# Kernel optimization log

Hardware: AMD Instinct MI355X
Metric: run time of the kernel (lower is better)

The kernel has to match this reference:

```python
import jax, jax.numpy as jnp
import numpy as np

N_NODES = 100000
N_EDGES = 1600000
N_GRAPHS = 64
VOCAB = 50000
D = 128
EPS = 1e-5


def setup_inputs() -> dict:
    key = jax.random.key(0)
    ks = jax.random.split(key, 24)
    tokens = jax.random.randint(ks[0], (N_NODES,), 0, VOCAB)
    src = jax.random.randint(ks[1], (N_EDGES,), 0, N_NODES)
    dst = jax.random.randint(ks[2], (N_EDGES,), 0, N_NODES)
    graph_ids = jnp.sort(jax.random.randint(ks[3], (N_NODES,), 0, N_GRAPHS))
    s = 1.0 / np.sqrt(D)
    inp = {
        'tokens': tokens, 'src': src, 'dst': dst, 'graph_ids': graph_ids,
        'embed': jax.random.normal(ks[4], (VOCAB, D), jnp.float32),
        'W1': jax.random.normal(ks[5], (D, D), jnp.float32) * s,
        'b1': jnp.zeros((D,), jnp.float32),
        'g1': jnp.ones((D,), jnp.float32), 'be1': jnp.zeros((D,), jnp.float32),
        'W2': jax.random.normal(ks[6], (D, D), jnp.float32) * s,
        'b2': jnp.zeros((D,), jnp.float32),
        'g2': jnp.ones((D,), jnp.float32), 'be2': jnp.zeros((D,), jnp.float32),
        'W3': jax.random.normal(ks[7], (D, D), jnp.float32) * s,
        'b3': jnp.zeros((D,), jnp.float32),
        'g3': jnp.ones((D,), jnp.float32), 'be3': jnp.zeros((D,), jnp.float32),
        'fcW1': jax.random.normal(ks[8], (D, D // 2), jnp.float32) * s,
        'fcb1': jnp.zeros((D // 2,), jnp.float32),
        'fcW2': jax.random.normal(ks[9], (D // 2, 2), jnp.float32) * (1.0 / np.sqrt(D // 2)),
        'fcb2': jnp.zeros((2,), jnp.float32),
    }
    return inp


def _graph_conv(h, src, dst, norm_src, norm_dst, W, b):
    # DGL GraphConv, norm='both': D_out^{-1/2} -> sum-aggregate -> D_in^{-1/2} -> linear
    msg = (h * norm_src[:, None])[src]                      # [E, D]
    agg = jax.ops.segment_sum(msg, dst, num_segments=N_NODES)
    return (agg * norm_dst[:, None]) @ W + b


def _bn_relu(h, gamma, beta):
    mu = jnp.mean(h, axis=0)
    var = jnp.mean((h - mu) ** 2, axis=0)                   # biased var (torch BN)
    return jax.nn.relu((h - mu) * jax.lax.rsqrt(var + EPS) * gamma + beta)


def reference(tokens, src, dst, graph_ids, embed,
              W1, b1, g1, be1, W2, b2, g2, be2, W3, b3, g3, be3,
              fcW1, fcb1, fcW2, fcb2):
    ones_e = jnp.ones((N_EDGES,), jnp.float32)
    deg_out = jnp.maximum(jax.ops.segment_sum(ones_e, src, num_segments=N_NODES), 1.0)
    deg_in = jnp.maximum(jax.ops.segment_sum(ones_e, dst, num_segments=N_NODES), 1.0)
    norm_src = jax.lax.rsqrt(deg_out)
    norm_dst = jax.lax.rsqrt(deg_in)

    h = embed[tokens]                                        # [N, D]
    h = _bn_relu(_graph_conv(h, src, dst, norm_src, norm_dst, W1, b1), g1, be1)
    h = _bn_relu(_graph_conv(h, src, dst, norm_src, norm_dst, W2, b2), g2, be2)
    h = _bn_relu(_graph_conv(h, src, dst, norm_src, norm_dst, W3, b3), g3, be3)

    # dgl.mean_nodes per graph
    sums = jax.ops.segment_sum(h, graph_ids, num_segments=N_GRAPHS)  # [G, D]
    cnts = jnp.maximum(jax.ops.segment_sum(jnp.ones((N_NODES,), jnp.float32), graph_ids, num_segments=N_GRAPHS), 1.0)
    hg = sums / cnts[:, None]

    hg = jax.nn.relu(hg @ fcW1 + fcb1)                       # dropout = identity (eval)
    return hg @ fcW2 + fcb2                                  # [G, 2]
```

## Files before the change

### kernel.cpp

```cpp
#include <hip/hip_runtime.h>

#define N_NODES 100000
#define N_EDGES 1600000
#define N_GRAPHS 64
#define DIM 128
#define BN_EPS 1e-5f
#define EPAD 2000000

#define NB_DEG 6250
#define NB_EMB 6250
#define NB_SENT 977
#define NB_WPREP 192
#define NB_HIST 391
#define NBUCK 782
#define NG (NBUCK * NB_HIST)
#define NB_SCANG 1195
#define BUCK_RESERVE 388

#define AT_STRIDE 136

typedef unsigned short ushort_t;
typedef unsigned char uchar_t;
typedef unsigned int uint_t;
typedef __attribute__((ext_vector_type(8))) short bf16x8;
typedef __attribute__((ext_vector_type(4))) float f32x4;

__device__ __forceinline__ float bfl(uint_t u) {
    union { uint_t i; float f; } v; v.i = u << 16; return v.f;
}
__device__ __forceinline__ float bfh(uint_t u) {
    union { uint_t i; float f; } v; v.i = u & 0xffff0000u; return v.f;
}
__device__ __forceinline__ ushort_t f2bf(float f) {
    union { float f; uint_t i; } v; v.f = f;
    uint_t x = v.i;
    return (ushort_t)((x + 0x7fffu + ((x >> 16) & 1u)) >> 16);
}
__device__ __forceinline__ uint_t pack2(float lo, float hi) {
    return ((uint_t)f2bf(hi) << 16) | (uint_t)f2bf(lo);
}

__global__ void k_zero(int* __restrict__ p, int n) {
    int i = blockIdx.x * blockDim.x + threadIdx.x;
    if (i < n) p[i] = 0;
}

__global__ void k_front(const int* __restrict__ src, const int* __restrict__ dst,
                        int* __restrict__ dego,
                        const int* __restrict__ tokens, const float* __restrict__ embed,
                        ushort_t* __restrict__ bufH, ushort_t* __restrict__ bufA,
                        int* __restrict__ esrc,
                        const float* __restrict__ w1, const float* __restrict__ w2,
                        const float* __restrict__ w3, ushort_t* __restrict__ wbt,
                        int* __restrict__ G) {
    __shared__ int hh[NBUCK];
    int b = blockIdx.x;
    int t = threadIdx.x;
    if (b < NB_DEG) {
        int e = b * 256 + t;
        if (e < N_EDGES) atomicAdd(&dego[src[e]], 1);
        return;
    }
    b -= NB_DEG;
    if (b < NB_EMB) {
        int gid = b * 256 + t;
        int node = gid >> 4, sub = gid & 15;
        const float* ep = embed + (size_t)tokens[node] * DIM + sub * 8;
        float4 a = *(const float4*)ep;
        float4 c = *(const float4*)(ep + 4);
        uint4 o;
        o.x = pack2(a.x, a.y); o.y = pack2(a.z, a.w);
        o.z = pack2(c.x, c.y); o.w = pack2(c.z, c.w);
        *(uint4*)(bufH + (size_t)node * DIM + sub * 8) = o;
        return;
    }
    b -= NB_EMB;
    if (b < NB_SENT) {
        int i0 = (b * 256 + t) * 8;
        int4 sv = make_int4(N_NODES, N_NODES, N_NODES, N_NODES);
        if (i0 + 8 <= EPAD) {
            *(int4*)(esrc + i0) = sv;
            *(int4*)(esrc + i0 + 4) = sv;
        } else {
            for (int i = i0; i < EPAD; ++i) esrc[i] = N_NODES;
        }
        if (b == 0 && t < 64)
            ((uint_t*)(bufA + (size_t)N_NODES * DIM))[t] = 0u;
        return;
    }
    b -= NB_SENT;
    if (b < NB_WPREP) {
        int i = b * 256 + t;
        int l = i >> 14;
        int idx = i & (DIM * DIM - 1);
        int n = idx >> 7, k = idx & (DIM - 1);
        const float* wsrc = (l == 0) ? w1 : (l == 1) ? w2 : w3;
        wbt[i] = f2bf(wsrc[k * DIM + n]);
        return;
    }
    b -= NB_WPREP;
    {
        for (int k = t; k < NBUCK; k += 256) hh[k] = 0;
        __syncthreads();
        int e0 = b * 4096;
        int e1 = min(e0 + 4096, N_EDGES);
        for (int i = e0 + t; i < e1; i += 256) atomicAdd(&hh[dst[i] >> 7], 1);
        __syncthreads();
        for (int k = t; k < NBUCK; k += 256) G[k * NB_HIST + b] = hh[k];
    }
}

__global__ void k_scanA(const int* __restrict__ G, int* __restrict__ Gs,
                        int* __restrict__ partials) {
    __shared__ int s[256];
    int t = threadIdx.x;
    int i = blockIdx.x * 256 + t;
    int v = (i < NG) ? G[i] : 0;
    s[t] = v;
    __syncthreads();
    for (int off = 1; off < 256; off <<= 1) {
        int add = (t >= off) ? s[t - off] : 0;
        __syncthreads();
        s[t] += add;
        __syncthreads();
    }
    if (i < NG) Gs[i + 1] = s[t];
    if (t == 255) partials[blockIdx.x] = s[t];
}

__global__ void k_scanB(const int* __restrict__ partials, int* __restrict__ Gs) {
    __shared__ int s[256];
    int t = threadIdx.x;
    int p = 0;
    for (int j = t; j < (int)blockIdx.x; j += 256) p += partials[j];
    s[t] = p;
    __syncthreads();
    for (int off = 128; off > 0; off >>= 1) {
        if (t < off) s[t] += s[t + off];
        __syncthreads();
    }
    int prefix = s[0];
    int i = blockIdx.x * 256 + t;
    if (i < NG) Gs[i + 1] += prefix;
    if (blockIdx.x == 0 && t == 0) Gs[0] = 0;
}

__global__ void k_pass2(const int* __restrict__ src, const int* __restrict__ dst,
                        const int* __restrict__ Gs, int* __restrict__ Csrc,
                        uchar_t* __restrict__ Cdl) {
    __shared__ int cur[NBUCK];
    int b = blockIdx.x;
    int t = threadIdx.x;
    for (int k = t; k < NBUCK; k += 256) cur[k] = Gs[k * NB_HIST + b];
    __syncthreads();
    int e0 = b * 4096;
    int e1 = min(e0 + 4096, N_EDGES);
    for (int i = e0 + t; i < e1; i += 256) {
        int d = dst[i];
        int slot = atomicAdd(&cur[d >> 7], 1);
        Csrc[slot] = src[i];
        Cdl[slot] = (uchar_t)(d & 127);
    }
}

__global__ void k_fine(const int* __restrict__ Csrc, const uchar_t* __restrict__ Cdl,
                       const int* __restrict__ Gs, const int* __restrict__ dego,
                       int* __restrict__ esrc, int* __restrict__ rowptr,
                       int* __restrict__ pdeg, float* __restrict__ ns,
                       float* __restrict__ nd) {
    __shared__ int hcnt[128];
    __shared__ int hstart[128];
    int k = blockIdx.x;
    int t = threadIdx.x;
    int node0 = k * 128;
    int nn = min(128, N_NODES - node0);
    int S = Gs[k * NB_HIST];
    int E = Gs[(k + 1) * NB_HIST];
    if (t < 128) hcnt[t] = 0;
    __syncthreads();
    for (int i = S + t; i < E; i += 256) atomicAdd(&hcnt[Cdl[i]], 1);
    __syncthreads();
    if (t == 0) {
        int acc = 0;
        for (int n = 0; n < nn; ++n) {
            hstart[n] = acc;
            acc += (hcnt[n] + 3) & ~3;
        }
    }
    __syncthreads();
    int base = (k * BUCK_RESERVE + S + 3) & ~3;
    if (t < nn) {
        int node = node0 + t;
        rowptr[node] = base + hstart[t];
        pdeg[node] = (hcnt[t] + 3) & ~3;
        nd[node] = rsqrtf(fmaxf((float)hcnt[t], 1.0f));
        ns[node] = rsqrtf(fmaxf((float)dego[node], 1.0f));
    }
    if (k == 0 && t == 0) ns[N_NODES] = 0.f;
    __syncthreads();
    for (int i = S + t; i < E; i += 256) {
        int slot = atomicAdd(&hstart[Cdl[i]], 1);
        esrc[base + slot] = Csrc[i];
    }
}

template <int DOBN>
__global__ void k_prescale(const ushort_t* __restrict__ yin, const float* __restrict__ ns,
                           const float* __restrict__ bnsum, const float* __restrict__ bnsq,
                           const float* __restrict__ g, const float* __restrict__ be,
                           ushort_t* __restrict__ xout) {
    __shared__ float sa[DIM], sc[DIM];
    int t = threadIdx.x;
    if (DOBN) {
        if (t < DIM) {
            float mu = bnsum[t] * (1.0f / N_NODES);
            float var = bnsq[t] * (1.0f / N_NODES) - mu * mu;
            float rstd = rsqrtf(var + BN_EPS);
            float a = g[t] * rstd;
            sa[t] = a;
            sc[t] = be[t] - mu * a;
        }
        __syncthreads();
    }
    int gid = blockIdx.x * 256 + t;
    int node = gid >> 4, sub = gid & 15;
    float s = ns[node];
    uint4 u = *(const uint4*)(yin + (size_t)node * DIM + sub * 8);
    float v[8] = {bfl(u.x), bfh(u.x), bfl(u.y), bfh(u.y),
                  bfl(u.z), bfh(u.z), bfl(u.w), bfh(u.w)};
    if (DOBN) {
        const float* a = sa + sub * 8;
        const float* c = sc + sub * 8;
#pragma unroll
        for (int i = 0; i < 8; ++i) v[i] = fmaxf(fmaf(v[i], a[i], c[i]), 0.f);
    }
#pragma unroll
    for (int i = 0; i < 8; ++i) v[i] *= s;
    uint4 o;
    o.x = pack2(v[0], v[1]); o.y = pack2(v[2], v[3]);
    o.z = pack2(v[4], v[5]); o.w = pack2(v[6], v[7]);
    *(uint4*)(xout + (size_t)node * DIM + sub * 8) = o;
}

__global__ __launch_bounds__(256) void k_agggemm(const ushort_t* __restrict__ hs,
        const int* __restrict__ rowptr, const int* __restrict__ pdeg,
        const int* __restrict__ esrc, const float* __restrict__ nd,
        const ushort_t* __restrict__ wbt, const float* __restrict__ bias,
        ushort_t* __restrict__ y,
        float* __restrict__ bnsum, float* __restrict__ bnsq) {
    __shared__ ushort_t at[64 * AT_STRIDE];
    __shared__ float csum[4][DIM], csq[4][DIM];
    int tid = threadIdx.x;
    int wave = tid >> 6;
    int lane = tid & 63;
    csum[wave][lane] = 0.f;
    csum[wave][lane + 64] = 0.f;
    csq[wave][lane] = 0.f;
    csq[wave][lane + 64] = 0.f;

    int bnode = blockIdx.x * 64 + wave * 16;
    int off = lane * 2;

    int rpv = 0, pdv = 0;
    if (lane < 16) {
        int nnode = bnode + lane;
        if (nnode < N_NODES) { rpv = rowptr[nnode]; pdv = pdeg[nnode]; }
    }

#define LD2(s) (*(const uint_t*)(hs + (size_t)(s) * DIM + off))
#define ACC8(I0, I1, X0, Y0, X1, Y1)                                           \
    {                                                                          \
        uint_t u0 = LD2(I0.x), u1 = LD2(I0.y), u2 = LD2(I0.z), u3 = LD2(I0.w); \
        uint_t u4 = LD2(I1.x), u5 = LD2(I1.y), u6 = LD2(I1.z), u7 = LD2(I1.w); \
        X0 += bfl(u0); Y0 += bfh(u0); X1 += bfl(u1); Y1 += bfh(u1);            \
        X0 += bfl(u2); Y0 += bfh(u2); X1 += bfl(u3); Y1 += bfh(u3);            \
        X0 += bfl(u4); Y0 += bfh(u4); X1 += bfl(u5); Y1 += bfh(u5);            \
        X0 += bfl(u6); Y0 += bfh(u6); X1 += bfl(u7); Y1 += bfh(u7);            \
    }
#define ACC4(I0, X0, Y0, X1, Y1)                                               \
    {                                                                          \
        uint_t u0 = LD2(I0.x), u1 = LD2(I0.y), u2 = LD2(I0.z), u3 = LD2(I0.w); \
        X0 += bfl(u0); Y0 += bfh(u0); X1 += bfl(u1); Y1 += bfh(u1);            \
        X0 += bfl(u2); Y0 += bfh(u2); X1 += bfl(u3); Y1 += bfh(u3);            \
    }

    for (int i = 0; i < 16; i += 2) {
        int nodeA = bnode + i;
        int nodeB = bnode + i + 1;
        int eA = __shfl(rpv, i);
        int endA = eA + __shfl(pdv, i);
        int eB = __shfl(rpv, i + 1);
        int endB = eB + __shfl(pdv, i + 1);
        float xA0 = 0.f, yA0 = 0.f, xA1 = 0.f, yA1 = 0.f;
        float xB0 = 0.f, yB0 = 0.f, xB1 = 0.f, yB1 = 0.f;
        if (eA + 8 <= endA && eB + 8 <= endB) {
            int4 cA0 = *(const int4*)(esrc + eA);
            int4 cA1 = *(const int4*)(esrc + eA + 4);
            int4 cB0 = *(const int4*)(esrc + eB);
            int4 cB1 = *(const int4*)(esrc + eB + 4);
            while (true) {
                int4 nA0 = *(const int4*)(esrc + eA + 8);
                int4 nA1 = *(const int4*)(esrc + eA + 12);
                int4 nB0 = *(const int4*)(esrc + eB + 8);
                int4 nB1 = *(const int4*)(esrc + eB + 12);
                ACC8(cA0, cA1, xA0, yA0, xA1, yA1);
                ACC8(cB0, cB1, xB0, yB0, xB1, yB1);
                eA += 8; eB += 8;
                if (!(eA + 8 <= endA && eB + 8 <= endB)) break;
                cA0 = nA0; cA1 = nA1; cB0 = nB0; cB1 = nB1;
            }
        }
        for (; eA + 8 <= endA; eA += 8) {
            int4 i0 = *(const int4*)(esrc + eA);
            int4 i1 = *(const int4*)(esrc + eA + 4);
            ACC8(i0, i1, xA0, yA0, xA1, yA1);
        }
        if (eA < endA) {
            int4 i0 = *(const int4*)(esrc + eA);
            ACC4(i0, xA0, yA0, xA1, yA1);
        }
        for (; eB + 8 <= endB; eB += 8) {
            int4 i0 = *(const int4*)(esrc + eB);
            int4 i1 = *(const int4*)(esrc + eB + 4);
            ACC8(i0, i1, xB0, yB0, xB1, yB1);
        }
        if (eB < endB) {
            int4 i0 = *(const int4*)(esrc + eB);
            ACC4(i0, xB0, yB0, xB1, yB1);
        }
        uint_t ovA = 0u, ovB = 0u;
        if (nodeA < N_NODES) {
            float n = nd[nodeA];
            ovA = pack2((xA0 + xA1) * n, (yA0 + yA1) * n);
        }
        if (nodeB < N_NODES) {
            float n = nd[nodeB];
            ovB = pack2((xB0 + xB1) * n, (yB0 + yB1) * n);
        }
        *(uint_t*)&at[(wave * 16 + i) * AT_STRIDE + off] = ovA;
        *(uint_t*)&at[(wave * 16 + i + 1) * AT_STRIDE + off] = ovB;
    }
#undef ACC8
#undef ACC4
#undef LD2

    int m16 = lane & 15;
    int quad = lane >> 4;
    f32x4 acc[8];
#pragma unroll
    for (int nb = 0; nb < 8; ++nb) acc[nb] = (f32x4)(0.f);

    const ushort_t* ap = &at[(wave * 16 + m16) * AT_STRIDE + quad * 8];
#pragma unroll
    for (int k0b = 0; k0b < 4; ++k0b) {
        bf16x8 af = *(const bf16x8*)(ap + k0b * 32);
#pragma unroll
        for (int nb = 0; nb < 8; ++nb) {
            int ncol = nb * 16 + m16;
            bf16x8 bfg = *(const bf16x8*)(wbt + (size_t)ncol * DIM + k0b * 32 + quad * 8);
            acc[nb] = __builtin_amdgcn_mfma_f32_16x16x32_bf16(af, bfg, acc[nb], 0, 0, 0);
        }
    }

#pragma unroll
    for (int nb = 0; nb < 8; ++nb) {
        int col = nb * 16 + m16;
        float bcol = bias[col];
        float ps = 0.f, pq = 0.f;
#pragma unroll
        for (int reg = 0; reg < 4; ++reg) {
            int r = bnode + quad * 4 + reg;
            if (r < N_NODES) {
                float v = acc[nb][reg] + bcol;
                ps += v; pq += v * v;
                y[(size_t)r * DIM + col] = f2bf(v);
            }
        }
        atomicAdd(&csum[wave][col], ps);
        atomicAdd(&csq[wave][col], pq);
    }
    __syncthreads();
    if (tid < DIM) {
        float s = csum[0][tid] + csum[1][tid] + csum[2][tid] + csum[3][tid];
        float q = csq[0][tid] + csq[1][tid] + csq[2][tid] + csq[3][tid];
        atomicAdd(&bnsum[tid], s);
        atomicAdd(&bnsq[tid], q);
    }
}

#define POOL_NODES 128
__global__ void k_pool(const ushort_t* __restrict__ yin, const int* __restrict__ gids,
                       const float* __restrict__ bnsum, const float* __restrict__ bnsq,
                       const float* __restrict__ g, const float* __restrict__ be,
                       float* __restrict__ pool, int* __restrict__ cnt) {
    __shared__ int h[N_GRAPHS];
    int col = threadIdx.x;
    float mu = bnsum[col] * (1.0f / N_NODES);
    float var = bnsq[col] * (1.0f / N_NODES) - mu * mu;
    float rstd = rsqrtf(var + BN_EPS);
    float a = g[col] * rstd;
    float c = be[col] - mu * a;
    if (col < N_GRAPHS) h[col] = 0;
    __syncthreads();
    int base = blockIdx.x * POOL_NODES;
    int end = min(base + POOL_NODES, N_NODES);
    for (int n = base + col; n < end; n += 128) atomicAdd(&h[gids[n]], 1);
    __syncthreads();
    if (col < N_GRAPHS && h[col]) atomicAdd(&cnt[col], h[col]);
    float acc = 0.f;
    int cur = gids[base];
    for (int n = base; n < end; ++n) {
        int gg = gids[n];
        if (gg != cur) {
            atomicAdd(&pool[(size_t)cur * DIM + col], acc);
            acc = 0.f;
            cur = gg;
        }
        uint_t u = *(const uint_t*)(yin + (size_t)n * DIM + (col & ~1));
        float v = (col & 1) ? bfh(u) : bfl(u);
        acc += fmaxf(fmaf(v, a, c), 0.f);
    }
    atomicAdd(&pool[(size_t)cur * DIM + col], acc);
}

__global__ void k_final(const float* __restrict__ pool, const int* __restrict__ cnt,
                        const float* __restrict__ fcW1, const float* __restrict__ fcb1,
                        const float* __restrict__ fcW2, const float* __restrict__ fcb2,
                        float* __restrict__ out) {
    __shared__ float hg[DIM];
    __shared__ float z[64];
    int g = blockIdx.x;
    int t = threadIdx.x;
    float cf = fmaxf((float)cnt[g], 1.0f);
    hg[t] = pool[(size_t)g * DIM + t] / cf;
    __syncthreads();
    if (t < 64) {
        float acc = fcb1[t];
        for (int k = 0; k < DIM; ++k)
            acc += hg[k] * fcW1[k * 64 + t];
        z[t] = fmaxf(acc, 0.f);
    }
    __syncthreads();
    if (t < 2) {
        float acc = fcb2[t];
        for (int k = 0; k < 64; ++k)
            acc += z[k] * fcW2[k * 2 + t];
        out[g * 2 + t] = acc;
    }
}

extern "C" void kernel_launch(void* const* d_in, const int* in_sizes, int n_in,
                              void* d_out, int out_size, void* d_ws, size_t ws_size,
                              hipStream_t stream) {
    const int* tokens = (const int*)d_in[0];
    const int* src = (const int*)d_in[1];
    const int* dst = (const int*)d_in[2];
    const int* gids = (const int*)d_in[3];
    const float* embed = (const float*)d_in[4];
    const float* W1 = (const float*)d_in[5];
    const float* b1 = (const float*)d_in[6];
    const float* g1 = (const float*)d_in[7];
    const float* be1 = (const float*)d_in[8];
    const float* W2 = (const float*)d_in[9];
    const float* b2 = (const float*)d_in[10];
    const float* g2 = (const float*)d_in[11];
    const float* be2 = (const float*)d_in[12];
    const float* W3 = (const float*)d_in[13];
    const float* b3 = (const float*)d_in[14];
    const float* g3 = (const float*)d_in[15];
    const float* be3 = (const float*)d_in[16];
    const float* fcW1 = (const float*)d_in[17];
    const float* fcb1 = (const float*)d_in[18];
    const float* fcW2 = (const float*)d_in[19];
    const float* fcb2 = (const float*)d_in[20];
    float* out = (float*)d_out;

    char* w = (char*)d_ws;
    auto alloc = [&](size_t bytes) {
        void* p = (void*)w;
        w += (bytes + 255) & ~(size_t)255;
        return p;
    };
    ushort_t* bufH = (ushort_t*)alloc((size_t)(N_NODES + 1) * DIM * 2);
    ushort_t* bufA = (ushort_t*)alloc((size_t)(N_NODES + 1) * DIM * 2);
    ushort_t* bufY = (ushort_t*)alloc((size_t)(N_NODES + 1) * DIM * 2);
    int* esrc = (int*)alloc((size_t)EPAD * 4);
    int* rowptr = (int*)alloc((size_t)N_NODES * 4);
    int* pdeg = (int*)alloc((size_t)N_NODES * 4);
    float* ns = (float*)alloc((size_t)(N_NODES + 1) * 4);
    float* nd = (float*)alloc((size_t)N_NODES * 4);
    ushort_t* wbt = (ushort_t*)alloc(3 * DIM * DIM * 2);
    int* G = (int*)alloc((size_t)NG * 4);
    int* Gs = (int*)alloc((size_t)(NG + 1) * 4);
    int* partials = (int*)alloc(2048 * 4);
    int* Csrc = (int*)alloc((size_t)N_EDGES * 4);
    uchar_t* Cdl = (uchar_t*)alloc((size_t)N_EDGES);
    char* zstart = w;
    int* dego = (int*)alloc((size_t)N_NODES * 4);
    float* bnsum = (float*)alloc(3 * DIM * 4);
    float* bnsq = (float*)alloc(3 * DIM * 4);
    float* pool = (float*)alloc((size_t)N_GRAPHS * DIM * 4);
    int* cnt = (int*)alloc((size_t)N_GRAPHS * 4);
    int zwords = (int)((size_t)(w - zstart) / 4);

    k_zero<<<(zwords + 255) / 256, 256, 0, stream>>>((int*)zstart, zwords);
    k_front<<<NB_DEG + NB_EMB + NB_SENT + NB_WPREP + NB_HIST, 256, 0, stream>>>(
        src, dst, dego, tokens, embed, bufH, bufA, esrc, W1, W2, W3, wbt, G);
    k_scanA<<<NB_SCANG, 256, 0, stream>>>(G, Gs, partials);
    k_scanB<<<NB_SCANG, 256, 0, stream>>>(partials, Gs);
    k_pass2<<<NB_HIST, 256, 0, stream>>>(src, dst, Gs, Csrc, Cdl);
    k_fine<<<NBUCK, 256, 0, stream>>>(Csrc, Cdl, Gs, dego, esrc, rowptr, pdeg, ns, nd);

    int nb_fused = (N_NODES + 63) / 64;
    int nb_ps = 6250;

    k_prescale<0><<<nb_ps, 256, 0, stream>>>(bufH, ns, nullptr, nullptr, nullptr, nullptr, bufA);
    k_agggemm<<<nb_fused, 256, 0, stream>>>(bufA, rowptr, pdeg, esrc, nd,
                                            wbt, b1, bufY, bnsum, bnsq);
    k_prescale<1><<<nb_ps, 256, 0, stream>>>(bufY, ns, bnsum, bnsq, g1, be1, bufA);
    k_agggemm<<<nb_fused, 256, 0, stream>>>(bufA, rowptr, pdeg, esrc, nd,
                                            wbt + (size_t)DIM * DIM, b2, bufH,
                                            bnsum + DIM, bnsq + DIM);
    k_prescale<1><<<nb_ps, 256, 0, stream>>>(bufH, ns, bnsum + DIM, bnsq + DIM, g2, be2, bufA);
    k_agggemm<<<nb_fused, 256, 0, stream>>>(bufA, rowptr, pdeg, esrc, nd,
                                            wbt + (size_t)2 * DIM * DIM, b3, bufY,
                                            bnsum + 2 * DIM, bnsq + 2 * DIM);

    k_pool<<<(N_NODES + POOL_NODES - 1) / POOL_NODES, DIM, 0, stream>>>(
        bufY, gids, bnsum + 2 * DIM, bnsq + 2 * DIM, g3, be3, pool, cnt);
    k_final<<<N_GRAPHS, DIM, 0, stream>>>(pool, cnt, fcW1, fcb1, fcW2, fcb2, out);
}
```

Before: 688.4 us.

## Compute out-degree via bucketed LDS histogram instead of global atomics

```diff
diff --git a/kernel.cpp b/kernel.cpp
--- a/kernel.cpp
+++ b/kernel.cpp
@@ -7,14 +7,13 @@
 #define BN_EPS 1e-5f
 #define EPAD 2000000
 
-#define NB_DEG 6250
 #define NB_EMB 6250
 #define NB_SENT 977
 #define NB_WPREP 192
 #define NB_HIST 391
 #define NBUCK 782
 #define NG (NBUCK * NB_HIST)
-#define NB_SCANG 1195
+#define NB_SCANG2 2389
 #define BUCK_RESERVE 388
 
 #define AT_STRIDE 136
@@ -46,22 +45,16 @@
 }
 
 __global__ void k_front(const int* __restrict__ src, const int* __restrict__ dst,
-                        int* __restrict__ dego,
                         const int* __restrict__ tokens, const float* __restrict__ embed,
                         ushort_t* __restrict__ bufH, ushort_t* __restrict__ bufA,
                         int* __restrict__ esrc,
                         const float* __restrict__ w1, const float* __restrict__ w2,
                         const float* __restrict__ w3, ushort_t* __restrict__ wbt,
-                        int* __restrict__ G) {
+                        int* __restrict__ GG) {
     __shared__ int hh[NBUCK];
+    __shared__ int hh2[NBUCK];
     int b = blockIdx.x;
     int t = threadIdx.x;
-    if (b < NB_DEG) {
-        int e = b * 256 + t;
-        if (e < N_EDGES) atomicAdd(&dego[src[e]], 1);
-        return;
-    }
-    b -= NB_DEG;
     if (b < NB_EMB) {
         int gid = b * 256 + t;
         int node = gid >> 4, sub = gid & 15;
@@ -100,22 +93,28 @@
     }
     b -= NB_WPREP;
     {
-        for (int k = t; k < NBUCK; k += 256) hh[k] = 0;
+        for (int k = t; k < NBUCK; k += 256) { hh[k] = 0; hh2[k] = 0; }
         __syncthreads();
         int e0 = b * 4096;
         int e1 = min(e0 + 4096, N_EDGES);
-        for (int i = e0 + t; i < e1; i += 256) atomicAdd(&hh[dst[i] >> 7], 1);
-        __syncthreads();
-        for (int k = t; k < NBUCK; k += 256) G[k * NB_HIST + b] = hh[k];
-    }
-}
-
-__global__ void k_scanA(const int* __restrict__ G, int* __restrict__ Gs,
+        for (int i = e0 + t; i < e1; i += 256) {
+            atomicAdd(&hh[dst[i] >> 7], 1);
+            atomicAdd(&hh2[src[i] >> 7], 1);
+        }
+        __syncthreads();
+        for (int k = t; k < NBUCK; k += 256) {
+            GG[k * NB_HIST + b] = hh[k];
+            GG[NG + k * NB_HIST + b] = hh2[k];
+        }
+    }
+}
+
+__global__ void k_scanA(const int* __restrict__ GG, int* __restrict__ Gs,
                         int* __restrict__ partials) {
     __shared__ int s[256];
     int t = threadIdx.x;
     int i = blockIdx.x * 256 + t;
-    int v = (i < NG) ? G[i] : 0;
+    int v = (i < 2 * NG) ? GG[i] : 0;
     s[t] = v;
     __syncthreads();
     for (int off = 1; off < 256; off <<= 1) {
@@ -124,7 +123,7 @@
         s[t] += add;
         __syncthreads();
     }
-    if (i < NG) Gs[i + 1] = s[t];
+    if (i < 2 * NG) Gs[i + 1] = s[t];
     if (t == 255) partials[blockIdx.x] = s[t];
 }
 
@@ -141,66 +140,87 @@
     }
     int prefix = s[0];
     int i = blockIdx.x * 256 + t;
-    if (i < NG) Gs[i + 1] += prefix;
+    if (i < 2 * NG) Gs[i + 1] += prefix;
     if (blockIdx.x == 0 && t == 0) Gs[0] = 0;
 }
 
 __global__ void k_pass2(const int* __restrict__ src, const int* __restrict__ dst,
                         const int* __restrict__ Gs, int* __restrict__ Csrc,
-                        uchar_t* __restrict__ Cdl) {
+                        uchar_t* __restrict__ Cdl, uchar_t* __restrict__ Cls) {
     __shared__ int cur[NBUCK];
+    __shared__ int cur2[NBUCK];
     int b = blockIdx.x;
     int t = threadIdx.x;
-    for (int k = t; k < NBUCK; k += 256) cur[k] = Gs[k * NB_HIST + b];
+    for (int k = t; k < NBUCK; k += 256) {
+        cur[k] = Gs[k * NB_HIST + b];
+        cur2[k] = Gs[NG + k * NB_HIST + b] - N_EDGES;
+    }
     __syncthreads();
     int e0 = b * 4096;
     int e1 = min(e0 + 4096, N_EDGES);
     for (int i = e0 + t; i < e1; i += 256) {
         int d = dst[i];
+        int s = src[i];
         int slot = atomicAdd(&cur[d >> 7], 1);
-        Csrc[slot] = src[i];
+        Csrc[slot] = s;
         Cdl[slot] = (uchar_t)(d & 127);
+        int slot2 = atomicAdd(&cur2[s >> 7], 1);
+        Cls[slot2] = (uchar_t)(s & 127);
     }
 }
 
 __global__ void k_fine(const int* __restrict__ Csrc, const uchar_t* __restrict__ Cdl,
-                       const int* __restrict__ Gs, const int* __restrict__ dego,
+                       const uchar_t* __restrict__ Cls, const int* __restrict__ Gs,
                        int* __restrict__ esrc, int* __restrict__ rowptr,
                        int* __restrict__ pdeg, float* __restrict__ ns,
                        float* __restrict__ nd) {
     __shared__ int hcnt[128];
     __shared__ int hstart[128];
-    int k = blockIdx.x;
-    int t = threadIdx.x;
-    int node0 = k * 128;
-    int nn = min(128, N_NODES - node0);
-    int S = Gs[k * NB_HIST];
-    int E = Gs[(k + 1) * NB_HIST];
-    if (t < 128) hcnt[t] = 0;
-    __syncthreads();
-    for (int i = S + t; i < E; i += 256) atomicAdd(&hcnt[Cdl[i]], 1);
-    __syncthreads();
-    if (t == 0) {
-        int acc = 0;
-        for (int n = 0; n < nn; ++n) {
-            hstart[n] = acc;
-            acc += (hcnt[n] + 3) & ~3;
-        }
-    }
-    __syncthreads();
-    int base = (k * BUCK_RESERVE + S + 3) & ~3;
-    if (t < nn) {
-        int node = node0 + t;
-        rowptr[node] = base + hstart[t];
-        pdeg[node] = (hcnt[t] + 3) & ~3;
-        nd[node] = rsqrtf(fmaxf((float)hcnt[t], 1.0f));
-        ns[node] = rsqrtf(fmaxf((float)dego[node], 1.0f));
-    }
-    if (k == 0 && t == 0) ns[N_NODES] = 0.f;
-    __syncthreads();
-    for (int i = S + t; i < E; i += 256) {
-        int slot = atomicAdd(&hstart[Cdl[i]], 1);
-        esrc[base + slot] = Csrc[i];
+    int b = blockIdx.x;
+    int t = threadIdx.x;
+    if (b < NBUCK) {
+        int k = b;
+        int node0 = k * 128;
+        int nn = min(128, N_NODES - node0);
+        int S = Gs[k * NB_HIST];
+        int E = Gs[(k + 1) * NB_HIST];
+        if (t < 128) hcnt[t] = 0;
+        __syncthreads();
+        for (int i = S + t; i < E; i += 256) atomicAdd(&hcnt[Cdl[i]], 1);
+        __syncthreads();
+        if (t == 0) {
+            int acc = 0;
+            for (int n = 0; n < nn; ++n) {
+                hstart[n] = acc;
+                acc += (hcnt[n] + 3) & ~3;
+            }
+        }
+        __syncthreads();
+        int base = (k * BUCK_RESERVE + S + 3) & ~3;
+        if (t < nn) {
+            int node = node0 + t;
+            rowptr[node] = base + hstart[t];
+            pdeg[node] = (hcnt[t] + 3) & ~3;
+            nd[node] = rsqrtf(fmaxf((float)hcnt[t], 1.0f));
+        }
+        __syncthreads();
+        for (int i = S + t; i < E; i += 256) {
+            int slot = atomicAdd(&hstart[Cdl[i]], 1);
+            esrc[base + slot] = Csrc[i];
+        }
+    } else {
+        int k = b - NBUCK;
+        int node0 = k * 128;
+        int nn = min(128, N_NODES - node0);
+        int S = Gs[NG + k * NB_HIST] - N_EDGES;
+        int E = Gs[NG + (k + 1) * NB_HIST] - N_EDGES;
+        if (t < 128) hcnt[t] = 0;
+        __syncthreads();
+        for (int i = S + t; i < E; i += 256) atomicAdd(&hcnt[Cls[i]], 1);
+        __syncthreads();
+        if (t < nn)
+            ns[node0 + t] = rsqrtf(fmaxf((float)hcnt[t], 1.0f));
+        if (k == 0 && t == 0) ns[N_NODES] = 0.f;
     }
 }
 
@@ -490,13 +510,13 @@
     float* ns = (float*)alloc((size_t)(N_NODES + 1) * 4);
     float* nd = (float*)alloc((size_t)N_NODES * 4);
     ushort_t* wbt = (ushort_t*)alloc(3 * DIM * DIM * 2);
-    int* G = (int*)alloc((size_t)NG * 4);
-    int* Gs = (int*)alloc((size_t)(NG + 1) * 4);
-    int* partials = (int*)alloc(2048 * 4);
+    int* GG = (int*)alloc((size_t)(2 * NG) * 4);
+    int* Gs = (int*)alloc((size_t)(2 * NG + 1) * 4);
+    int* partials = (int*)alloc(4096 * 4);
     int* Csrc = (int*)alloc((size_t)N_EDGES * 4);
     uchar_t* Cdl = (uchar_t*)alloc((size_t)N_EDGES);
+    uchar_t* Cls = (uchar_t*)alloc((size_t)N_EDGES);
     char* zstart = w;
-    int* dego = (int*)alloc((size_t)N_NODES * 4);
     float* bnsum = (float*)alloc(3 * DIM * 4);
     float* bnsq = (float*)alloc(3 * DIM * 4);
     float* pool = (float*)alloc((size_t)N_GRAPHS * DIM * 4);
@@ -504,12 +524,12 @@
     int zwords = (int)((size_t)(w - zstart) / 4);
 
     k_zero<<<(zwords + 255) / 256, 256, 0, stream>>>((int*)zstart, zwords);
-    k_front<<<NB_DEG + NB_EMB + NB_SENT + NB_WPREP + NB_HIST, 256, 0, stream>>>(
-        src, dst, dego, tokens, embed, bufH, bufA, esrc, W1, W2, W3, wbt, G);
-    k_scanA<<<NB_SCANG, 256, 0, stream>>>(G, Gs, partials);
-    k_scanB<<<NB_SCANG, 256, 0, stream>>>(partials, Gs);
-    k_pass2<<<NB_HIST, 256, 0, stream>>>(src, dst, Gs, Csrc, Cdl);
-    k_fine<<<NBUCK, 256, 0, stream>>>(Csrc, Cdl, Gs, dego, esrc, rowptr, pdeg, ns, nd);
+    k_front<<<NB_EMB + NB_SENT + NB_WPREP + NB_HIST, 256, 0, stream>>>(
+        src, dst, tokens, embed, bufH, bufA, esrc, W1, W2, W3, wbt, GG);
+    k_scanA<<<NB_SCANG2, 256, 0, stream>>>(GG, Gs, partials);
+    k_scanB<<<NB_SCANG2, 256, 0, stream>>>(partials, Gs);
+    k_pass2<<<NB_HIST, 256, 0, stream>>>(src, dst, Gs, Csrc, Cdl, Cls);
+    k_fine<<<2 * NBUCK, 256, 0, stream>>>(Csrc, Cdl, Cls, Gs, esrc, rowptr, pdeg, ns, nd);
 
     int nb_fused = (N_NODES + 63) / 64;
     int nb_ps = 6250;
```

Result: faster. 668.0 us (-3.0%).
